# Kernel optimization log

Measured on AMD Instinct MI355X. Metric: run time of the kernel, lower is better.

Reference implementation:

```python
import jax, jax.numpy as jnp
import numpy as np

D_MODEL = 1024
D_STATE = 16
D_CONV = 4
EXPAND = 2
HEADDIM = 8
D_INNER = EXPAND * D_MODEL            # 2048
NHEADS = D_INNER // HEADDIM           # 256
CONV_DIM = D_INNER + 2 * D_STATE      # 2080 (ngroups=1)
D_IN_PROJ = 2 * D_INNER + 2 * D_STATE + NHEADS  # 4384
B_SZ, SEQ = 4, 2048
EPS = 1e-5


def setup_inputs() -> dict:
    key = jax.random.key(0)
    ks = jax.random.split(key, 8)
    return {
        "x": jax.random.normal(ks[0], (B_SZ, SEQ, D_MODEL), jnp.float32),
        "ln_w": jnp.ones((D_MODEL,), jnp.float32),
        "ln_b": jnp.zeros((D_MODEL,), jnp.float32),
        "W_in": jax.random.normal(ks[1], (D_MODEL, D_IN_PROJ), jnp.float32) * 0.02,
        "conv_w": jax.random.normal(ks[2], (D_CONV, 1, CONV_DIM), jnp.float32) * 0.2,
        "conv_b": jnp.zeros((CONV_DIM,), jnp.float32),
        "A_log": jnp.log(jax.random.uniform(ks[3], (NHEADS,), jnp.float32, 1.0, 16.0)),
        "Dp": jnp.ones((NHEADS,), jnp.float32) + 0.1 * jax.random.normal(ks[4], (NHEADS,), jnp.float32),
        "dt_bias": 0.5 * jax.random.normal(ks[5], (NHEADS,), jnp.float32),
        "rms_w": jnp.ones((D_INNER,), jnp.float32),
        "W_out": jax.random.normal(ks[6], (D_INNER, D_MODEL), jnp.float32) * 0.02,
    }


def _mamba_block(x, ln_w, ln_b, W_in, conv_w, conv_b, A_log, Dp, dt_bias, rms_w, W_out):
    B, L, _ = x.shape
    # pre-norm LayerNorm
    mu = jnp.mean(x, axis=-1, keepdims=True)
    var = jnp.mean((x - mu) ** 2, axis=-1, keepdims=True)
    xn = (x - mu) * jax.lax.rsqrt(var + EPS) * ln_w + ln_b

    # in_proj -> z, xBC, dt
    u = xn @ W_in                                    # (B, L, 4384)
    z = u[..., :D_INNER]
    xBC = u[..., D_INNER:D_INNER + CONV_DIM]
    dt = jax.nn.softplus(u[..., -NHEADS:] + dt_bias)  # (B, L, NHEADS)

    # causal depthwise conv1d + SiLU
    xp = jnp.pad(xBC, ((0, 0), (D_CONV - 1, 0), (0, 0)))
    xBC = jax.lax.conv_general_dilated(
        xp, conv_w, window_strides=(1,), padding="VALID",
        dimension_numbers=("NWC", "WIO", "NWC"), feature_group_count=CONV_DIM)
    xBC = jax.nn.silu(xBC + conv_b)

    xs = xBC[..., :D_INNER].reshape(B, L, NHEADS, HEADDIM)   # SSM input
    Bm = xBC[..., D_INNER:D_INNER + D_STATE]                  # (B, L, N)
    Cm = xBC[..., D_INNER + D_STATE:]                          # (B, L, N)

    A = -jnp.exp(A_log)                                       # (NHEADS,)

    def step(h, inp):
        # h: (B, H, P, N)
        x_t, B_t, C_t, dt_t = inp
        dA = jnp.exp(dt_t * A)                                 # (B, H)
        h = h * dA[..., None, None] + jnp.einsum("bh,bhp,bn->bhpn", dt_t, x_t, B_t)
        y = jnp.einsum("bhpn,bn->bhp", h, C_t)
        return h, y

    h0 = jnp.zeros((B, NHEADS, HEADDIM, D_STATE), x.dtype)
    _, ys = jax.lax.scan(step, h0, (xs.swapaxes(0, 1), Bm.swapaxes(0, 1),
                                     Cm.swapaxes(0, 1), dt.swapaxes(0, 1)))
    y = ys.swapaxes(0, 1) + Dp[None, None, :, None] * xs       # (B, L, H, P)
    y = y.reshape(B, L, D_INNER)

    # gated RMSNorm: rmsnorm(y * silu(z)) * weight
    g = y * jax.nn.silu(z)
    g = g * jax.lax.rsqrt(jnp.mean(g * g, axis=-1, keepdims=True) + EPS) * rms_w

    return x + g @ W_out


def reference(x, ln_w, ln_b, W_in, conv_w, conv_b, A_log, Dp, dt_bias, rms_w, W_out):
    return _mamba_block(x, ln_w, ln_b, W_in, conv_w, conv_b, A_log, Dp, dt_bias, rms_w, W_out)
```

## Files before the change

### kernel.cpp

```cpp
#include <hip/hip_runtime.h>

typedef __bf16 bf16;
typedef __attribute__((ext_vector_type(8))) __bf16 bf16x8;
typedef __attribute__((ext_vector_type(4))) float f32x4;

#define B_SZ 4
#define SEQ 2048
#define DM 1024
#define DIN 2048
#define NH 256
#define DSTATE 16
#define CONVD 2080
#define DPROJ 4384
#define NPAD1 4608
#define MROWS 8192
#define NC 64
#define LC 32
#define UROWB 8768

__device__ __forceinline__ void gload_lds16(const void* g, void* l) {
  __builtin_amdgcn_global_load_lds(
      (__attribute__((address_space(1))) void*)g,
      (__attribute__((address_space(3))) void*)l, 16, 0, 0);
}

template <int N>
__device__ __forceinline__ void vm_wait() {
  asm volatile("s_waitcnt vmcnt(%0)" ::"n"(N) : "memory");
}
__device__ __forceinline__ void bar() { asm volatile("s_barrier" ::: "memory"); }
__device__ __forceinline__ void lgkm0() {
  asm volatile("s_waitcnt lgkmcnt(0)" ::: "memory");
}

__global__ void transpose_cvt(const float* __restrict__ W, bf16* __restrict__ WT,
                              int K, int N, int Npad) {
  __shared__ float tile[32][33];
  int k0 = blockIdx.x * 32, n0 = blockIdx.y * 32;
  int tx = threadIdx.x, ty = threadIdx.y;
#pragma unroll
  for (int j = 0; j < 4; j++) {
    int k = k0 + ty + 8 * j, n = n0 + tx;
    tile[ty + 8 * j][tx] = (k < K && n < N) ? W[(size_t)k * N + n] : 0.f;
  }
  __syncthreads();
#pragma unroll
  for (int j = 0; j < 4; j++) {
    int n = n0 + ty + 8 * j, k = k0 + tx;
    if (n < Npad && k < K) WT[(size_t)n * K + k] = (bf16)tile[tx][ty + 8 * j];
  }
}

__global__ __launch_bounds__(256) void ln_kernel(const float* __restrict__ x,
                                                 const float* __restrict__ lw,
                                                 const float* __restrict__ lb,
                                                 bf16* __restrict__ xn) {
  int row = blockIdx.x;
  int t = threadIdx.x;
  f32x4 v4 = ((const f32x4*)(x + (size_t)row * DM))[t];
  float v0 = v4[0], v1 = v4[1], v2 = v4[2], v3 = v4[3];
  float s = v0 + v1 + v2 + v3;
  float s2 = v0 * v0 + v1 * v1 + v2 * v2 + v3 * v3;
#pragma unroll
  for (int off = 32; off > 0; off >>= 1) {
    s += __shfl_down(s, off);
    s2 += __shfl_down(s2, off);
  }
  __shared__ float ps[8];
  int wave = t >> 6, lane = t & 63;
  if (lane == 0) { ps[wave] = s; ps[4 + wave] = s2; }
  __syncthreads();
  s = ps[0] + ps[1] + ps[2] + ps[3];
  s2 = ps[4] + ps[5] + ps[6] + ps[7];
  float mean = s * (1.f / DM);
  float var = s2 * (1.f / DM) - mean * mean;
  float rstd = rsqrtf(var + 1e-5f);
  f32x4 wv = ((const f32x4*)lw)[t];
  f32x4 bv = ((const f32x4*)lb)[t];
  bf16 o[4];
  o[0] = (bf16)((v0 - mean) * rstd * wv[0] + bv[0]);
  o[1] = (bf16)((v1 - mean) * rstd * wv[1] + bv[1]);
  o[2] = (bf16)((v2 - mean) * rstd * wv[2] + bv[2]);
  o[3] = (bf16)((v3 - mean) * rstd * wv[3] + bv[3]);
  bf16* dst = xn + (size_t)row * DM + t * 4;
  dst[0] = o[0]; dst[1] = o[1]; dst[2] = o[2]; dst[3] = o[3];
}

__global__ __launch_bounds__(512, 2) void gemm1_8p(const bf16* __restrict__ A,
                                                   const bf16* __restrict__ BT,
                                                   bf16* __restrict__ C) {
  __shared__ char lds[147456];
  int bid = blockIdx.x;
  int swz = (bid & 7) * 96 + (bid >> 3);
  int bm = swz / 24, bn = swz - (swz / 24) * 24;
  int m0 = bm * 256, n0 = bn * 192;
  int t = threadIdx.x, lane = t & 63, wave = t >> 6;
  int wm = wave >> 2, wn = wave & 3;
  int lr16 = lane & 15, kq = lane >> 4;
  int ts0 = kq ^ (lr16 & 7);
  int ts1 = (4 + kq) ^ (lr16 & 7);
  int sw = (lane & 7) ^ (lane >> 3);
  int l8 = lane >> 3;
  const char* Ab = (const char*)A;
  const char* Bb = (const char*)BT;

  auto stA = [&](int kt, int ab) {
    char* slot = lds + ab * 32768;
    size_t ko = (size_t)kt * 128 + sw * 16;
#pragma unroll
    for (int g = 0; g < 4; g++) {
      int c = wave * 4 + g;
      gload_lds16(Ab + (size_t)(m0 + c * 8 + l8) * 2048 + ko, slot + c * 1024);
    }
  };
  auto stB = [&](int kt, int p) {
    char* slot = lds + 98304 + p * 24576;
    size_t ko = (size_t)kt * 128 + sw * 16;
#pragma unroll
    for (int g = 0; g < 3; g++) {
      int c = wave * 3 + g;
      gload_lds16(Bb + (size_t)(n0 + c * 8 + l8) * 2048 + ko, slot + c * 1024);
    }
  };

  f32x4 acc[8][3] = {};
  bf16x8 a_[4][2], b_[3][2];

  stA(0, 0); stB(0, 0); stA(1, 1);
  vm_wait<4>();
  bar();
#pragma unroll 1
  for (int kt = 0; kt < 16; kt++) {
    int ab = kt % 3;
    int p = kt & 1;
    {
      const char* sa = lds + ab * 32768;
      const char* sb = lds + 98304 + p * 24576;
#pragma unroll
      for (int mi = 0; mi < 4; mi++) {
        int lrow = wm * 128 + mi * 16 + lr16;
        a_[mi][0] = *(const bf16x8*)(sa + lrow * 128 + ts0 * 16);
        a_[mi][1] = *(const bf16x8*)(sa + lrow * 128 + ts1 * 16);
      }
#pragma unroll
      for (int ni = 0; ni < 3; ni++) {
        int lrow = wn * 48 + ni * 16 + lr16;
        b_[ni][0] = *(const bf16x8*)(sb + lrow * 128 + ts0 * 16);
        b_[ni][1] = *(const bf16x8*)(sb + lrow * 128 + ts1 * 16);
      }
      if (kt < 15) stB(kt + 1, p ^ 1);
      if (kt < 14) stA(kt + 2, (kt + 2) % 3);
      bar();
      lgkm0();
      __builtin_amdgcn_s_setprio(1);
#pragma unroll
      for (int mi = 0; mi < 4; mi++)
#pragma unroll
        for (int ni = 0; ni < 3; ni++) {
          acc[mi][ni] = __builtin_amdgcn_mfma_f32_16x16x32_bf16(a_[mi][0], b_[ni][0], acc[mi][ni], 0, 0, 0);
          acc[mi][ni] = __builtin_amdgcn_mfma_f32_16x16x32_bf16(a_[mi][1], b_[ni][1], acc[mi][ni], 0, 0, 0);
        }
      __builtin_amdgcn_s_setprio(0);
      bar();
    }
    {
      const char* sa = lds + ab * 32768;
#pragma unroll
      for (int mi = 0; mi < 4; mi++) {
        int lrow = wm * 128 + 64 + mi * 16 + lr16;
        a_[mi][0] = *(const bf16x8*)(sa + lrow * 128 + ts0 * 16);
        a_[mi][1] = *(const bf16x8*)(sa + lrow * 128 + ts1 * 16);
      }
      if (kt < 14) vm_wait<4>();
      else if (kt == 14) vm_wait<0>();
      bar();
      lgkm0();
      __builtin_amdgcn_s_setprio(1);
#pragma unroll
      for (int mi = 0; mi < 4; mi++)
#pragma unroll
        for (int ni = 0; ni < 3; ni++) {
          acc[4 + mi][ni] = __builtin_amdgcn_mfma_f32_16x16x32_bf16(a_[mi][0], b_[ni][0], acc[4 + mi][ni], 0, 0, 0);
          acc[4 + mi][ni] = __builtin_amdgcn_mfma_f32_16x16x32_bf16(a_[mi][1], b_[ni][1], acc[4 + mi][ni], 0, 0, 0);
        }
      __builtin_amdgcn_s_setprio(0);
      bar();
    }
  }
#pragma unroll
  for (int fr = 0; fr < 8; fr++)
#pragma unroll
    for (int ni = 0; ni < 3; ni++) {
      int row = m0 + wm * 128 + fr * 16 + kq * 4;
      int col = n0 + wn * 48 + ni * 16 + lr16;
      f32x4 v = acc[fr][ni];
      if (col < 4384) {
#pragma unroll
        for (int r = 0; r < 4; r++)
          C[(size_t)(row + r) * DPROJ + col] = (bf16)v[r];
      }
    }
}

#define G2_PHASE(MQ, P, STAGE, VMW)                                                        \
  {                                                                                        \
    const char* sa_ = lds + ((P) * 2 + (MQ)) * 16384;                                      \
    const char* sb_ = lds + 65536 + (P) * 16384;                                           \
    bf16x8 a_[4][2], b_[2][2];                                                             \
    _Pragma("unroll") for (int mi = 0; mi < 4; mi++) {                                     \
      int lrow = wm * 64 + mi * 16 + lr16;                                                 \
      a_[mi][0] = *(const bf16x8*)(sa_ + lrow * 128 + ts0 * 16);                           \
      a_[mi][1] = *(const bf16x8*)(sa_ + lrow * 128 + ts1 * 16);                           \
    }                                                                                      \
    _Pragma("unroll") for (int ni = 0; ni < 2; ni++) {                                     \
      int lrow = wn * 32 + ni * 16 + lr16;                                                 \
      b_[ni][0] = *(const bf16x8*)(sb_ + lrow * 128 + ts0 * 16);                           \
      b_[ni][1] = *(const bf16x8*)(sb_ + lrow * 128 + ts1 * 16);                           \
    }                                                                                      \
    STAGE;                                                                                 \
    VMW;                                                                                   \
    bar();                                                                                 \
    lgkm0();                                                                               \
    __builtin_amdgcn_s_setprio(1);                                                         \
    _Pragma("unroll") for (int mi = 0; mi < 4; mi++)                                       \
      _Pragma("unroll") for (int ni = 0; ni < 2; ni++) {                                   \
        acc[(MQ) * 4 + mi][ni] = __builtin_amdgcn_mfma_f32_16x16x32_bf16(                  \
            a_[mi][0], b_[ni][0], acc[(MQ) * 4 + mi][ni], 0, 0, 0);                        \
        acc[(MQ) * 4 + mi][ni] = __builtin_amdgcn_mfma_f32_16x16x32_bf16(                  \
            a_[mi][1], b_[ni][1], acc[(MQ) * 4 + mi][ni], 0, 0, 0);                        \
      }                                                                                    \
    __builtin_amdgcn_s_setprio(0);                                                         \
    bar();                                                                                 \
  }

__global__ __launch_bounds__(512, 2) void gemm2_8p(const bf16* __restrict__ A,
                                                   const bf16* __restrict__ BT,
                                                   float* __restrict__ C,
                                                   const float* __restrict__ Xres) {
  __shared__ char lds[98304];
  int bid = blockIdx.x;
  int swz = (bid & 7) * 32 + (bid >> 3);
  int bm = swz >> 3, bn = swz & 7;
  int m0 = bm * 256, n0 = bn * 128;
  int t = threadIdx.x, lane = t & 63, wave = t >> 6;
  int wm = wave >> 2, wn = wave & 3;
  int lr16 = lane & 15, kq = lane >> 4;
  int ts0 = kq ^ (lr16 & 7);
  int ts1 = (4 + kq) ^ (lr16 & 7);
  int sw = (lane & 7) ^ ((lane >> 3) & 7);
  int l8 = lane >> 3;
  int c0 = 2 * wave, c1 = 2 * wave + 1;
  int lr0 = c0 * 8 + l8, lr1 = c1 * 8 + l8;
  const char* Ab = (const char*)A;
  const char* Bb = (const char*)BT;
  int grA0 = m0 + (lr0 >> 6) * 128 + (lr0 & 63);
  int grA1 = m0 + (lr1 >> 6) * 128 + (lr1 & 63);
  int gcB0 = n0 + lr0, gcB1 = n0 + lr1;

  auto stA = [&](int kt, int p, int mq) {
    char* slot = lds + (p * 2 + mq) * 16384;
    size_t ko = (size_t)kt * 128 + sw * 16;
    gload_lds16(Ab + (size_t)(grA0 + mq * 64) * 4096 + ko, slot + c0 * 1024);
    gload_lds16(Ab + (size_t)(grA1 + mq * 64) * 4096 + ko, slot + c1 * 1024);
  };
  auto stB = [&](int kt, int p) {
    char* slot = lds + 65536 + p * 16384;
    size_t ko = (size_t)kt * 128 + sw * 16;
    gload_lds16(Bb + (size_t)gcB0 * 4096 + ko, slot + c0 * 1024);
    gload_lds16(Bb + (size_t)gcB1 * 4096 + ko, slot + c1 * 1024);
  };

  f32x4 acc[8][2] = {};
  stA(0, 0, 0); stB(0, 0); stA(0, 0, 1); stA(1, 1, 0);
  vm_wait<4>();
  bar();
#pragma unroll 1
  for (int kt = 0; kt < 32; kt++) {
    int p = kt & 1;
    G2_PHASE(0, p, { if (kt + 1 < 32) { stB(kt + 1, p ^ 1); stA(kt + 1, p ^ 1, 1); } },
             { if (kt < 31) vm_wait<6>(); else vm_wait<0>(); });
    G2_PHASE(1, p, { if (kt + 2 < 32) stA(kt + 2, p, 0); },
             { if (kt < 30) vm_wait<4>(); else if (kt == 30) vm_wait<2>(); });
  }
#pragma unroll
  for (int mq = 0; mq < 2; mq++)
#pragma unroll
    for (int mi = 0; mi < 4; mi++)
#pragma unroll
      for (int ni = 0; ni < 2; ni++) {
        int row = m0 + wm * 128 + mq * 64 + mi * 16 + kq * 4;
        int col = n0 + wn * 32 + ni * 16 + lr16;
        f32x4 v = acc[mq * 4 + mi][ni];
#pragma unroll
        for (int r = 0; r < 4; r++) {
          size_t o = (size_t)(row + r) * DM + col;
          C[o] = Xres[o] + v[r];
        }
      }
}

__global__ __launch_bounds__(256) void conv_prep3(const bf16* __restrict__ u,
                                                  const float* __restrict__ cw,
                                                  const float* __restrict__ cb,
                                                  const float* __restrict__ dt_bias,
                                                  bf16* __restrict__ xs,
                                                  float* __restrict__ BC,
                                                  float* __restrict__ dtf) {
  const int JPR = 292;
  int idx = blockIdx.x * 256 + threadIdx.x;
  if (idx >= MROWS * JPR) return;
  int row = idx / JPR;
  int j = idx - row * JPR;
  int t = row & (SEQ - 1);
  if (j < 260) {
    int c0 = j * 8;
    float acc[8];
#pragma unroll
    for (int i = 0; i < 8; i++) acc[i] = cb[c0 + i];
    const bf16* ub = u + (size_t)row * DPROJ + DIN + c0;
#pragma unroll
    for (int tap = 0; tap < 4; tap++) {
      int tt = t - 3 + tap;
      if (tt >= 0) {
        bf16x8 uv = *(const bf16x8*)(ub + (ptrdiff_t)(tap - 3) * DPROJ);
        const float* wv = cw + tap * CONVD + c0;
#pragma unroll
        for (int i = 0; i < 8; i++) acc[i] += wv[i] * (float)uv[i];
      }
    }
    if (c0 < DIN) {
      bf16x8 o;
#pragma unroll
      for (int i = 0; i < 8; i++) {
        float sv = acc[i] / (1.f + __expf(-acc[i]));
        o[i] = (bf16)sv;
      }
      *(bf16x8*)(xs + (size_t)row * DIN + c0) = o;
    } else {
      float* bc = BC + (size_t)row * 32 + (c0 - DIN);
#pragma unroll
      for (int i = 0; i < 8; i++) bc[i] = acc[i] / (1.f + __expf(-acc[i]));
    }
  } else {
    int h0 = (j - 260) * 8;
    bf16x8 uv = *(const bf16x8*)(u + (size_t)row * DPROJ + (DPROJ - NH) + h0);
    float* dst = dtf + (size_t)row * NH + h0;
#pragma unroll
    for (int i = 0; i < 8; i++) {
      float xv = (float)uv[i] + dt_bias[h0 + i];
      dst[i] = (xv > 20.f) ? xv : log1pf(__expf(xv));
    }
  }
}

__global__ __launch_bounds__(64) void scan_p1(const bf16* __restrict__ xs,
                                              const float* __restrict__ BC,
                                              const float* __restrict__ dtf,
                                              const float* __restrict__ A_log,
                                              bf16* __restrict__ uscr) {
  int c = blockIdx.x & 63, hg = (blockIdx.x >> 6) & 31, b = blockIdx.x >> 11;
  int lane = threadIdx.x, hh = lane >> 3;
  int h = hg * 8 + hh;
  float A = -__expf(A_log[h]);
  float st[16];
#pragma unroll
  for (int n = 0; n < 16; n++) st[n] = 0.f;
  float pcum = 1.f;
  size_t rb = (size_t)b * SEQ + (size_t)c * LC;
  for (int t = 0; t < LC; t++) {
    size_t row = rb + t;
    const float* bcrow = BC + row * 32;
    float dtv = dtf[row * NH + h];
    float x = (float)xs[row * DIN + hg * 64 + lane];
    float dA = __expf(dtv * A);
    pcum *= dA;
    float w = dtv * x;
#pragma unroll
    for (int n = 0; n < 16; n++) st[n] = st[n] * dA + w * bcrow[n];
  }
  char* slot = (char*)uscr + (size_t)blockIdx.x * UROWB + 4096;
  float* S = (float*)slot;
#pragma unroll
  for (int n = 0; n < 16; n++) S[lane * 16 + n] = st[n];
  if ((lane & 7) == 0) ((float*)(slot + 4096))[hh] = pcum;
}

__global__ __launch_bounds__(64) void scan_p2(bf16* __restrict__ uscr) {
  int bh = blockIdx.x;
  int lane = threadIdx.x, hh = lane >> 3;
  float H[16];
#pragma unroll
  for (int n = 0; n < 16; n++) H[n] = 0.f;
  char* base = (char*)uscr + (size_t)bh * NC * UROWB + 4096;
  float sN[16], PN;
  {
    float* S = (float*)base;
#pragma unroll
    for (int n = 0; n < 16; n++) sN[n] = S[lane * 16 + n];
    PN = ((const float*)(base + 4096))[hh];
  }
  for (int c = 0; c < NC; c++) {
    float sC[16], PC = PN;
#pragma unroll
    for (int n = 0; n < 16; n++) sC[n] = sN[n];
    if (c + 1 < NC) {
      char* slot = base + (size_t)(c + 1) * UROWB;
      float* S = (float*)slot;
#pragma unroll
      for (int n = 0; n < 16; n++) sN[n] = S[lane * 16 + n];
      PN = ((const float*)(slot + 4096))[hh];
    }
    float* S0 = (float*)(base + (size_t)c * UROWB);
#pragma unroll
    for (int n = 0; n < 16; n++) {
      float hn = H[n];
      S0[lane * 16 + n] = hn;
      H[n] = PC * hn + sC[n];
    }
  }
}

__global__ __launch_bounds__(64) void scan_p3(const bf16* __restrict__ xs,
                                              const float* __restrict__ BC,
                                              const float* __restrict__ dtf,
                                              const float* __restrict__ A_log,
                                              const float* __restrict__ Dp,
                                              const bf16* __restrict__ uscr,
                                              bf16* __restrict__ y) {
  int c = blockIdx.x & 63, hg = (blockIdx.x >> 6) & 31, b = blockIdx.x >> 11;
  int lane = threadIdx.x, hh = lane >> 3;
  int h = hg * 8 + hh;
  float A = -__expf(A_log[h]);
  float D = Dp[h];
  const char* slot = (const char*)uscr + (size_t)blockIdx.x * UROWB + 4096;
  float st[16];
#pragma unroll
  for (int n = 0; n < 16; n++) st[n] = ((const float*)slot)[lane * 16 + n];
  size_t rb = (size_t)b * SEQ + (size_t)c * LC;
  for (int t = 0; t < LC; t++) {
    size_t row = rb + t;
    const float* bcrow = BC + row * 32;
    float dtv = dtf[row * NH + h];
    float x = (float)xs[row * DIN + hg * 64 + lane];
    float dA = __expf(dtv * A);
    float w = dtv * x;
    float yv = 0.f;
#pragma unroll
    for (int n = 0; n < 16; n++) {
      st[n] = st[n] * dA + w * bcrow[n];
      yv += st[n] * bcrow[16 + n];
    }
    y[row * DIN + hg * 64 + lane] = (bf16)(yv + D * x);
  }
}

__global__ __launch_bounds__(256) void gate_rms(const bf16* __restrict__ u,
                                                const bf16* __restrict__ y,
                                                const float* __restrict__ rms_w,
                                                bf16* __restrict__ g) {
  int row = blockIdx.x;
  int t = threadIdx.x;
  bf16x8 zv = ((const bf16x8*)(u + (size_t)row * DPROJ))[t];
  bf16x8 yv = ((const bf16x8*)(y + (size_t)row * DIN))[t];
  float gv[8];
  float s2 = 0.f;
#pragma unroll
  for (int i = 0; i < 8; i++) {
    float z = (float)zv[i];
    float yy = (float)yv[i];
    float gg = yy * z / (1.f + __expf(-z));
    gv[i] = gg;
    s2 += gg * gg;
  }
#pragma unroll
  for (int off = 32; off > 0; off >>= 1) s2 += __shfl_down(s2, off);
  __shared__ float ps[4];
  int wave = t >> 6, lane = t & 63;
  if (lane == 0) ps[wave] = s2;
  __syncthreads();
  s2 = ps[0] + ps[1] + ps[2] + ps[3];
  float scale = rsqrtf(s2 * (1.f / DIN) + 1e-5f);
  f32x4 w0 = ((const f32x4*)rms_w)[2 * t];
  f32x4 w1 = ((const f32x4*)rms_w)[2 * t + 1];
  bf16x8 og;
#pragma unroll
  for (int i = 0; i < 4; i++) og[i] = (bf16)(gv[i] * scale * w0[i]);
#pragma unroll
  for (int i = 0; i < 4; i++) og[4 + i] = (bf16)(gv[4 + i] * scale * w1[i]);
  ((bf16x8*)(g + (size_t)row * DIN))[t] = og;
}

extern "C" void kernel_launch(void* const* d_in, const int* in_sizes, int n_in,
                              void* d_out, int out_size, void* d_ws, size_t ws_size,
                              hipStream_t stream) {
  const float* x = (const float*)d_in[0];
  const float* lnw = (const float*)d_in[1];
  const float* lnb = (const float*)d_in[2];
  const float* Win = (const float*)d_in[3];
  const float* cw = (const float*)d_in[4];
  const float* cb = (const float*)d_in[5];
  const float* Alog = (const float*)d_in[6];
  const float* Dpv = (const float*)d_in[7];
  const float* dtb = (const float*)d_in[8];
  const float* rmsw = (const float*)d_in[9];
  const float* Wout = (const float*)d_in[10];
  float* out = (float*)d_out;

  char* ws = (char*)d_ws;
  bf16* u = (bf16*)(ws + 0);
  bf16* xnb = (bf16*)(ws + 71827456);
  bf16* WinT = (bf16*)(ws + 88604672);
  bf16* yb = (bf16*)(ws + 71827456);
  bf16* xsb = (bf16*)(ws + 105381888);
  bf16* gb = (bf16*)(ws + 105381888);
  float* BC = (float*)(ws + 138936320);
  float* dtf = (float*)(ws + 139984896);
  bf16* WoutT = (bf16*)(ws + 148373504);

  transpose_cvt<<<dim3(32, 144), dim3(32, 8), 0, stream>>>(Win, WinT, 1024, DPROJ, NPAD1);
  transpose_cvt<<<dim3(64, 32), dim3(32, 8), 0, stream>>>(Wout, WoutT, DIN, DM, DM);
  ln_kernel<<<MROWS, 256, 0, stream>>>(x, lnw, lnb, xnb);
  gemm1_8p<<<768, 512, 0, stream>>>(xnb, WinT, u);
  conv_prep3<<<(MROWS * 292) / 256, 256, 0, stream>>>(u, cw, cb, dtb, xsb, BC, dtf);
  scan_p1<<<MROWS, 64, 0, stream>>>(xsb, BC, dtf, Alog, u);
  scan_p2<<<128, 64, 0, stream>>>(u);
  scan_p3<<<MROWS, 64, 0, stream>>>(xsb, BC, dtf, Alog, Dpv, u, yb);
  gate_rms<<<MROWS, 256, 0, stream>>>(u, yb, rmsw, gb);
  gemm2_8p<<<256, 512, 0, stream>>>(gb, WoutT, out, x);
}
```

Measured before the change: 298.6 us.

## Swap A/B buffering depths in in_proj GEMM and remap tiles per XCD

The in_proj GEMM now double-buffers the A tile and triple-buffers the smaller B tile instead of the reverse, cutting shared memory from 144KB to 136KB. It prefetches B two k-steps ahead and A one step ahead, with the vmcnt waits adjusted to match. The block-to-tile mapping is changed so each XCD owns a contiguous group of M rows and cycles through N tiles, aiming for better L2 reuse of A. The A prefetch now has less lead time, so A load latency may be less well hidden.

Result: no change. 298.1 us (-0.2%).

```diff
diff --git a/kernel.cpp b/kernel.cpp
--- a/kernel.cpp
+++ b/kernel.cpp
@@ -89,10 +89,12 @@
 __global__ __launch_bounds__(512, 2) void gemm1_8p(const bf16* __restrict__ A,
                                                    const bf16* __restrict__ BT,
                                                    bf16* __restrict__ C) {
-  __shared__ char lds[147456];
+  __shared__ char lds[139264];
   int bid = blockIdx.x;
-  int swz = (bid & 7) * 96 + (bid >> 3);
-  int bm = swz / 24, bn = swz - (swz / 24) * 24;
+  int xcd = bid & 7;
+  int l = bid >> 3;
+  int bm = xcd * 4 + ((l >> 3) & 3);
+  int bn = (l >> 5) * 8 + (l & 7);
   int m0 = bm * 256, n0 = bn * 192;
   int t = threadIdx.x, lane = t & 63, wave = t >> 6;
   int wm = wave >> 2, wn = wave & 3;
@@ -104,8 +106,8 @@
   const char* Ab = (const char*)A;
   const char* Bb = (const char*)BT;
 
-  auto stA = [&](int kt, int ab) {
-    char* slot = lds + ab * 32768;
+  auto stA = [&](int kt) {
+    char* slot = lds + (kt & 1) * 32768;
     size_t ko = (size_t)kt * 128 + sw * 16;
 #pragma unroll
     for (int g = 0; g < 4; g++) {
@@ -113,8 +115,8 @@
       gload_lds16(Ab + (size_t)(m0 + c * 8 + l8) * 2048 + ko, slot + c * 1024);
     }
   };
-  auto stB = [&](int kt, int p) {
-    char* slot = lds + 98304 + p * 24576;
+  auto stB = [&](int kt) {
+    char* slot = lds + 65536 + (kt % 3) * 24576;
     size_t ko = (size_t)kt * 128 + sw * 16;
 #pragma unroll
     for (int g = 0; g < 3; g++) {
@@ -126,16 +128,14 @@
   f32x4 acc[8][3] = {};
   bf16x8 a_[4][2], b_[3][2];
 
-  stA(0, 0); stB(0, 0); stA(1, 1);
-  vm_wait<4>();
+  stA(0); stB(0); stA(1); stB(1);
+  vm_wait<7>();
   bar();
 #pragma unroll 1
   for (int kt = 0; kt < 16; kt++) {
-    int ab = kt % 3;
-    int p = kt & 1;
     {
-      const char* sa = lds + ab * 32768;
-      const char* sb = lds + 98304 + p * 24576;
+      const char* sa = lds + (kt & 1) * 32768;
+      const char* sb = lds + 65536 + (kt % 3) * 24576;
 #pragma unroll
       for (int mi = 0; mi < 4; mi++) {
         int lrow = wm * 128 + mi * 16 + lr16;
@@ -148,8 +148,8 @@
         b_[ni][0] = *(const bf16x8*)(sb + lrow * 128 + ts0 * 16);
         b_[ni][1] = *(const bf16x8*)(sb + lrow * 128 + ts1 * 16);
       }
-      if (kt < 15) stB(kt + 1, p ^ 1);
-      if (kt < 14) stA(kt + 2, (kt + 2) % 3);
+      if (kt >= 1 && kt < 15) stA(kt + 1);
+      if (kt < 14) stB(kt + 2);
       bar();
       lgkm0();
       __builtin_amdgcn_s_setprio(1);
@@ -164,14 +164,14 @@
       bar();
     }
     {
-      const char* sa = lds + ab * 32768;
+      const char* sa = lds + (kt & 1) * 32768;
 #pragma unroll
       for (int mi = 0; mi < 4; mi++) {
         int lrow = wm * 128 + 64 + mi * 16 + lr16;
         a_[mi][0] = *(const bf16x8*)(sa + lrow * 128 + ts0 * 16);
         a_[mi][1] = *(const bf16x8*)(sa + lrow * 128 + ts1 * 16);
       }
-      if (kt < 14) vm_wait<4>();
+      if (kt <= 13) vm_wait<3>();
       else if (kt == 14) vm_wait<0>();
       bar();
       lgkm0();
```
